# Kernel tuning notes

Hardware: AMD Instinct MI355X
Metric: run time of the kernel (lower is better)

## Reference

```python
import jax, jax.numpy as jnp
import numpy as np

N_NODES = 50000

def _sage_conv(x, src, dst, W_l, b_l, W_r):
    # PyG SAGEConv, aggr='mean': out = lin_l(mean_j x_j) + lin_r(x_i)
    msg = x[src]                                                 # [E, d] gather
    agg = jax.ops.segment_sum(msg, dst, num_segments=N_NODES)   # [N, d] scatter-add
    cnt = jax.ops.segment_sum(jnp.ones((src.shape[0], 1), x.dtype), dst,
                              num_segments=N_NODES)              # [N, 1] in-degree
    agg = agg / jnp.maximum(cnt, 1.0)                            # mean (0 for isolated nodes)
    return agg @ W_l + b_l + x @ W_r

def setup_inputs() -> dict:
    key = jax.random.key(0)
    ks = jax.random.split(key, 8)
    in_f, hid, out_f = 128, 128, 64
    E = 640000
    x = jax.random.normal(ks[0], (N_NODES, in_f), dtype=jnp.float32)
    edge_index = jax.random.randint(ks[1], (2, E), 0, N_NODES, dtype=jnp.int64)
    def glorot(k, fan_in, fan_out):
        lim = (6.0 / (fan_in + fan_out)) ** 0.5
        return jax.random.uniform(k, (fan_in, fan_out), jnp.float32, -lim, lim)
    return {
        "x": x,
        "edge_index": edge_index,
        "W1_l": glorot(ks[2], in_f, hid),
        "b1": jnp.zeros((hid,), jnp.float32),
        "W1_r": glorot(ks[3], in_f, hid),
        "W2_l": glorot(ks[4], hid, out_f),
        "b2": jnp.zeros((out_f,), jnp.float32),
        "W2_r": glorot(ks[5], hid, out_f),
    }

def reference(x, edge_index, W1_l, b1, W1_r, W2_l, b2, W2_r):
    src, dst = edge_index[0], edge_index[1]
    h = _sage_conv(x, src, dst, W1_l, b1, W1_r)
    h = jax.nn.relu(h)
    # dropout: eval mode -> identity (deterministic reference)
    h = _sage_conv(h, src, dst, W2_l, b2, W2_r)
    return h
```

## Files before the change

kernel.cpp:

```cpp
#include <hip/hip_runtime.h>
#include <cstddef>

static constexpr int N_NODES = 50000;
static constexpr int E_EDGES = 640000;
static constexpr int F = 128;
static constexpr int MAXD = 64;

typedef __bf16 b8 __attribute__((ext_vector_type(8)));
typedef float  f4 __attribute__((ext_vector_type(4)));
typedef float  f2 __attribute__((ext_vector_type(2)));

__device__ inline unsigned short f2bf(float f) {
    unsigned u = __float_as_uint(f);
    u += 0x7FFF + ((u >> 16) & 1);
    return (unsigned short)(u >> 16);
}
__device__ inline float bflo(unsigned u) { return __uint_as_float(u << 16); }
__device__ inline float bfhi(unsigned u) { return __uint_as_float(u & 0xFFFF0000u); }

__device__ inline void accq(float* s, uint2 u) {
    f2 p;
    p = __builtin_amdgcn_cvt_pk_f32_fp8(u.x, false); s[0] += p.x; s[1] += p.y;
    p = __builtin_amdgcn_cvt_pk_f32_fp8(u.x, true);  s[2] += p.x; s[3] += p.y;
    p = __builtin_amdgcn_cvt_pk_f32_fp8(u.y, false); s[4] += p.x; s[5] += p.y;
    p = __builtin_amdgcn_cvt_pk_f32_fp8(u.y, true);  s[6] += p.x; s[7] += p.y;
}
__device__ inline void accq16(float* s, uint4 u) {
    accq(s,     make_uint2(u.x, u.y));
    accq(s + 8, make_uint2(u.z, u.w));
}

template<int BN>
__device__ inline void pack_w_body(int t, const float* __restrict__ Wl,
                                   const float* __restrict__ Wr, uint4* __restrict__ Bp) {
    constexpr int NTg = BN / 16;
    int wid = t >> 6, lane = t & 63;
    if (wid >= 8 * NTg) return;
    int kq = lane >> 4, m = lane & 15;
    int kt = wid / NTg, nt = wid % NTg;
    unsigned short tmp[8];
#pragma unroll
    for (int j = 0; j < 8; ++j) {
        int k = kt * 32 + kq * 8 + j;
        const float* W = (k < 128) ? Wl : Wr;
        tmp[j] = f2bf(W[(size_t)(k & 127) * BN + nt * 16 + m]);
    }
    uint4 u;
    u.x = tmp[0] | ((unsigned)tmp[1] << 16);
    u.y = tmp[2] | ((unsigned)tmp[3] << 16);
    u.z = tmp[4] | ((unsigned)tmp[5] << 16);
    u.w = tmp[6] | ((unsigned)tmp[7] << 16);
    Bp[wid * 64 + lane] = u;
}

__global__ __launch_bounds__(256)
void prep(const int* __restrict__ ei, int* __restrict__ deg, int* __restrict__ col,
          const float* __restrict__ x, uint4* __restrict__ xb, uint2* __restrict__ xq,
          const float* __restrict__ W1l, const float* __restrict__ W1r, uint4* __restrict__ Bp1,
          const float* __restrict__ W2l, const float* __restrict__ W2r, uint4* __restrict__ Bp2) {
    int b = blockIdx.x, tid = threadIdx.x;
    if (b < 5000 && (b & 1) == 0) {
        int e = (b >> 1) * 256 + tid;
        int s = ei[e], d = ei[E_EDGES + e];
        int r = atomicAdd(&deg[d], 1);
        if (r < MAXD) col[(d << 6) + r] = s;
    } else if (b < 5625) {
        int ci = (b < 5000) ? (b >> 1) : (2500 + (b - 5000));
        int i = ci * 256 + tid;
        const float4* s = (const float4*)x + (size_t)i * 2;
        float4 v0 = s[0], v1 = s[1];
        uint4 u;
        u.x = f2bf(v0.x) | ((unsigned)f2bf(v0.y) << 16);
        u.y = f2bf(v0.z) | ((unsigned)f2bf(v0.w) << 16);
        u.z = f2bf(v1.x) | ((unsigned)f2bf(v1.y) << 16);
        u.w = f2bf(v1.z) | ((unsigned)f2bf(v1.w) << 16);
        xb[i] = u;
        uint2 q;
        q.x = __builtin_amdgcn_cvt_pk_fp8_f32(v0.x, v0.y, 0, false);
        q.x = __builtin_amdgcn_cvt_pk_fp8_f32(v0.z, v0.w, q.x, true);
        q.y = __builtin_amdgcn_cvt_pk_fp8_f32(v1.x, v1.y, 0, false);
        q.y = __builtin_amdgcn_cvt_pk_fp8_f32(v1.z, v1.w, q.y, true);
        xq[i] = q;
    } else if (b < 5641) {
        pack_w_body<128>((b - 5625) * 256 + tid, W1l, W1r, Bp1);
    } else {
        pack_w_body<64>((b - 5641) * 256 + tid, W2l, W2r, Bp2);
    }
}

__global__ __launch_bounds__(256)
void sage_l1(const uint2* __restrict__ featq,
             const unsigned short* __restrict__ featb,
             const int* __restrict__ deg,
             const int* __restrict__ col,
             const unsigned short* __restrict__ Bp1,
             const unsigned short* __restrict__ Bp2,
             const float* __restrict__ b1,
             const float* __restrict__ b2,
             unsigned char* __restrict__ Zq,
             float* __restrict__ out) {
    constexpr int LDW = 68;
    __shared__ unsigned Alds[16 * LDW];
    __shared__ unsigned short Hlds[16 * 136];

    const int tid  = threadIdx.x;
    const int wv   = tid >> 6;
    const int lane = tid & 63;
    const int c    = lane & 15;
    const int g    = lane >> 4;
    const int node0 = blockIdx.x * 16;
    const int node  = node0 + wv * 4 + g;

    {
        int d0 = deg[node];
        int d  = d0 < MAXD ? d0 : MAXD;
        int jb = node << 6, je = jb + d;
        float s0[8] = {0.f,0.f,0.f,0.f,0.f,0.f,0.f,0.f};
        float s1[8] = {0.f,0.f,0.f,0.f,0.f,0.f,0.f,0.f};
        float s2[8] = {0.f,0.f,0.f,0.f,0.f,0.f,0.f,0.f};
        float s3[8] = {0.f,0.f,0.f,0.f,0.f,0.f,0.f,0.f};
        int j = jb;
        for (; j + 7 < je; j += 8) {
            uint2 u0 = featq[(size_t)col[j + 0] * 16 + c];
            uint2 u1 = featq[(size_t)col[j + 1] * 16 + c];
            uint2 u2 = featq[(size_t)col[j + 2] * 16 + c];
            uint2 u3 = featq[(size_t)col[j + 3] * 16 + c];
            uint2 u4 = featq[(size_t)col[j + 4] * 16 + c];
            uint2 u5 = featq[(size_t)col[j + 5] * 16 + c];
            uint2 u6 = featq[(size_t)col[j + 6] * 16 + c];
            uint2 u7 = featq[(size_t)col[j + 7] * 16 + c];
            accq(s0, u0); accq(s1, u1); accq(s2, u2); accq(s3, u3);
            accq(s0, u4); accq(s1, u5); accq(s2, u6); accq(s3, u7);
        }
        if (j + 3 < je) {
            uint2 u0 = featq[(size_t)col[j + 0] * 16 + c];
            uint2 u1 = featq[(size_t)col[j + 1] * 16 + c];
            uint2 u2 = featq[(size_t)col[j + 2] * 16 + c];
            uint2 u3 = featq[(size_t)col[j + 3] * 16 + c];
            accq(s0, u0); accq(s1, u1); accq(s2, u2); accq(s3, u3);
            j += 4;
        }
        for (; j < je; ++j) {
            uint2 u0 = featq[(size_t)col[j] * 16 + c];
            accq(s0, u0);
        }
        float inv = 1.0f / (float)(d > 0 ? d : 1);
        float r[8];
#pragma unroll
        for (int k = 0; k < 8; ++k) r[k] = ((s0[k] + s1[k]) + (s2[k] + s3[k])) * inv;
        uint4 o;
        o.x = f2bf(r[0]) | ((unsigned)f2bf(r[1]) << 16);
        o.y = f2bf(r[2]) | ((unsigned)f2bf(r[3]) << 16);
        o.z = f2bf(r[4]) | ((unsigned)f2bf(r[5]) << 16);
        o.w = f2bf(r[6]) | ((unsigned)f2bf(r[7]) << 16);
        *((uint4*)&Alds[(wv * 4 + g) * LDW + c * 4]) = o;
    }
    __syncthreads();

    const int m  = lane & 15;
    const int kq = lane >> 4;
    const unsigned short* srow = featb + (size_t)(node0 + m) * F + kq * 8;

    f4 zero = {0.f, 0.f, 0.f, 0.f};
    f4 acc[2] = {zero, zero};
#pragma unroll
    for (int kt = 0; kt < 8; ++kt) {
        b8 a;
        if (kt < 4) a = *((const b8*)((const char*)Alds + m * 272 + kt * 64 + kq * 16));
        else        a = *((const b8*)(srow + (kt - 4) * 32));
#pragma unroll
        for (int t = 0; t < 2; ++t) {
            int nt = wv * 2 + t;
            b8 b = *((const b8*)(Bp1 + ((size_t)(kt * 8 + nt) * 64 + lane) * 8));
            acc[t] = __builtin_amdgcn_mfma_f32_16x16x32_bf16(a, b, acc[t], 0, 0, 0);
        }
    }
    {
        int rowb = kq * 4;
#pragma unroll
        for (int t = 0; t < 2; ++t) {
            int cc = (wv * 2 + t) * 16 + m;
            float bv = b1[cc];
#pragma unroll
            for (int r = 0; r < 4; ++r) {
                float v = fmaxf(acc[t][r] + bv, 0.0f);
                Hlds[(rowb + r) * 136 + cc] = f2bf(v);
            }
        }
    }
    __syncthreads();

    f4 accZ = zero, accS = zero;
#pragma unroll
    for (int kt = 0; kt < 4; ++kt) {
        b8 a = *((const b8*)((const char*)Hlds + m * 272 + kt * 64 + kq * 16));
        b8 bz = *((const b8*)(Bp2 + ((size_t)(kt * 4 + wv) * 64 + lane) * 8));
        b8 bs = *((const b8*)(Bp2 + ((size_t)((kt + 4) * 4 + wv) * 64 + lane) * 8));
        accZ = __builtin_amdgcn_mfma_f32_16x16x32_bf16(a, bz, accZ, 0, 0, 0);
        accS = __builtin_amdgcn_mfma_f32_16x16x32_bf16(a, bs, accS, 0, 0, 0);
    }
    {
        int rowg = node0 + kq * 4;
        int cc = wv * 16 + m;
        float bv = b2[cc];
#pragma unroll
        for (int r = 0; r < 4; ++r) {
            unsigned q = __builtin_amdgcn_cvt_pk_fp8_f32(accZ[r], accZ[r], 0, false);
            Zq[(size_t)(rowg + r) * 64 + cc] = (unsigned char)(q & 0xFF);
            out[(size_t)(rowg + r) * 64 + cc] = accS[r] + bv;
        }
    }
}

__global__ __launch_bounds__(256)
void gather_add(const uint4* __restrict__ Zq,
                const int* __restrict__ deg,
                const int* __restrict__ col,
                float* __restrict__ out, int N) {
    int t = blockIdx.x * 256 + threadIdx.x;
    int node = t >> 2;
    if (node >= N) return;
    int c = t & 3;

    int d0 = deg[node];
    int d  = d0 < MAXD ? d0 : MAXD;
    int jb = node << 6, je = jb + d;
    float s0[16] = {0.f,0.f,0.f,0.f,0.f,0.f,0.f,0.f,0.f,0.f,0.f,0.f,0.f,0.f,0.f,0.f};
    float s1[16] = {0.f,0.f,0.f,0.f,0.f,0.f,0.f,0.f,0.f,0.f,0.f,0.f,0.f,0.f,0.f,0.f};
    float s2[16] = {0.f,0.f,0.f,0.f,0.f,0.f,0.f,0.f,0.f,0.f,0.f,0.f,0.f,0.f,0.f,0.f};
    float s3[16] = {0.f,0.f,0.f,0.f,0.f,0.f,0.f,0.f,0.f,0.f,0.f,0.f,0.f,0.f,0.f,0.f};
    int j = jb;
    for (; j + 7 < je; j += 8) {
        uint4 u0 = Zq[(size_t)col[j + 0] * 4 + c];
        uint4 u1 = Zq[(size_t)col[j + 1] * 4 + c];
        uint4 u2 = Zq[(size_t)col[j + 2] * 4 + c];
        uint4 u3 = Zq[(size_t)col[j + 3] * 4 + c];
        uint4 u4 = Zq[(size_t)col[j + 4] * 4 + c];
        uint4 u5 = Zq[(size_t)col[j + 5] * 4 + c];
        uint4 u6 = Zq[(size_t)col[j + 6] * 4 + c];
        uint4 u7 = Zq[(size_t)col[j + 7] * 4 + c];
        accq16(s0, u0); accq16(s1, u1); accq16(s2, u2); accq16(s3, u3);
        accq16(s0, u4); accq16(s1, u5); accq16(s2, u6); accq16(s3, u7);
    }
    if (j + 3 < je) {
        uint4 u0 = Zq[(size_t)col[j + 0] * 4 + c];
        uint4 u1 = Zq[(size_t)col[j + 1] * 4 + c];
        uint4 u2 = Zq[(size_t)col[j + 2] * 4 + c];
        uint4 u3 = Zq[(size_t)col[j + 3] * 4 + c];
        accq16(s0, u0); accq16(s1, u1); accq16(s2, u2); accq16(s3, u3);
        j += 4;
    }
    for (; j < je; ++j) {
        uint4 u0 = Zq[(size_t)col[j] * 4 + c];
        accq16(s0, u0);
    }
    float inv = 1.0f / (float)(d > 0 ? d : 1);
    float* op = out + (size_t)node * 64 + c * 16;
#pragma unroll
    for (int q = 0; q < 4; ++q) {
        float4 o = *((float4*)(op + q * 4));
        o.x += ((s0[q*4+0] + s1[q*4+0]) + (s2[q*4+0] + s3[q*4+0])) * inv;
        o.y += ((s0[q*4+1] + s1[q*4+1]) + (s2[q*4+1] + s3[q*4+1])) * inv;
        o.z += ((s0[q*4+2] + s1[q*4+2]) + (s2[q*4+2] + s3[q*4+2])) * inv;
        o.w += ((s0[q*4+3] + s1[q*4+3]) + (s2[q*4+3] + s3[q*4+3])) * inv;
        *((float4*)(op + q * 4)) = o;
    }
}


extern "C" void kernel_launch(void* const* d_in, const int* in_sizes, int n_in,
                              void* d_out, int out_size, void* d_ws, size_t ws_size,
                              hipStream_t stream) {
    const float* x   = (const float*)d_in[0];
    const int*   ei  = (const int*)d_in[1];
    const float* W1l = (const float*)d_in[2];
    const float* b1  = (const float*)d_in[3];
    const float* W1r = (const float*)d_in[4];
    const float* W2l = (const float*)d_in[5];
    const float* b2  = (const float*)d_in[6];
    const float* W2r = (const float*)d_in[7];
    float* out = (float*)d_out;

    unsigned* Zq    = (unsigned*)d_ws;
    unsigned* xb    = Zq + (size_t)N_NODES * 16;
    unsigned* xq    = xb + (size_t)N_NODES * 64;
    unsigned* Bp1   = xq + (size_t)N_NODES * 32;
    unsigned* Bp2   = Bp1 + 16384;
    int* col        = (int*)(Bp2 + 8192);
    int* deg        = col + (size_t)N_NODES * MAXD;

    hipMemsetAsync(deg, 0, (size_t)N_NODES * sizeof(int), stream);

    prep<<<5649, 256, 0, stream>>>(ei, deg, col, x, (uint4*)xb, (uint2*)xq,
                                   W1l, W1r, (uint4*)Bp1, W2l, W2r, (uint4*)Bp2);

    sage_l1<<<N_NODES / 16, 256, 0, stream>>>(
        (const uint2*)xq, (const unsigned short*)xb, deg, col,
        (const unsigned short*)Bp1, (const unsigned short*)Bp2,
        b1, b2, (unsigned char*)Zq, out);

    gather_add<<<(N_NODES * 4 + 255) / 256, 256, 0, stream>>>(
        (const uint4*)Zq, deg, col, out, N_NODES);
}
```

Measured before the change: 171.0 us.

## Pad degree counters, batch edge atomics per thread, widen gather_add parallelism

Degree counters are now padded to one per 64 bytes (stride 16 ints) so concurrent atomics on neighboring nodes do not share cache lines. Each edge thread in prep now handles four edges, issuing all loads and then all atomics, and the prep grid is rebalanced to fit. gather_add uses 8 threads per node with 8-byte loads instead of 4 threads with 16-byte loads, which doubles thread-level parallelism for the latency-bound gather. The cost is a 16x larger degree buffer to memset and fewer bytes per load.

```diff
diff --git a/kernel.cpp b/kernel.cpp
--- a/kernel.cpp
+++ b/kernel.cpp
@@ -5,6 +5,7 @@
 static constexpr int E_EDGES = 640000;
 static constexpr int F = 128;
 static constexpr int MAXD = 64;
+static constexpr int DEGS = 16;
 
 typedef __bf16 b8 __attribute__((ext_vector_type(8)));
 typedef float  f4 __attribute__((ext_vector_type(4)));
@@ -15,8 +16,6 @@
     u += 0x7FFF + ((u >> 16) & 1);
     return (unsigned short)(u >> 16);
 }
-__device__ inline float bflo(unsigned u) { return __uint_as_float(u << 16); }
-__device__ inline float bfhi(unsigned u) { return __uint_as_float(u & 0xFFFF0000u); }
 
 __device__ inline void accq(float* s, uint2 u) {
     f2 p;
@@ -24,10 +23,6 @@
     p = __builtin_amdgcn_cvt_pk_f32_fp8(u.x, true);  s[2] += p.x; s[3] += p.y;
     p = __builtin_amdgcn_cvt_pk_f32_fp8(u.y, false); s[4] += p.x; s[5] += p.y;
     p = __builtin_amdgcn_cvt_pk_f32_fp8(u.y, true);  s[6] += p.x; s[7] += p.y;
-}
-__device__ inline void accq16(float* s, uint4 u) {
-    accq(s,     make_uint2(u.x, u.y));
-    accq(s + 8, make_uint2(u.z, u.w));
 }
 
 template<int BN>
@@ -59,32 +54,43 @@
           const float* __restrict__ W1l, const float* __restrict__ W1r, uint4* __restrict__ Bp1,
           const float* __restrict__ W2l, const float* __restrict__ W2r, uint4* __restrict__ Bp2) {
     int b = blockIdx.x, tid = threadIdx.x;
-    if (b < 5000 && (b & 1) == 0) {
-        int e = (b >> 1) * 256 + tid;
-        int s = ei[e], d = ei[E_EDGES + e];
-        int r = atomicAdd(&deg[d], 1);
-        if (r < MAXD) col[(d << 6) + r] = s;
-    } else if (b < 5625) {
-        int ci = (b < 5000) ? (b >> 1) : (2500 + (b - 5000));
-        int i = ci * 256 + tid;
-        const float4* s = (const float4*)x + (size_t)i * 2;
-        float4 v0 = s[0], v1 = s[1];
-        uint4 u;
-        u.x = f2bf(v0.x) | ((unsigned)f2bf(v0.y) << 16);
-        u.y = f2bf(v0.z) | ((unsigned)f2bf(v0.w) << 16);
-        u.z = f2bf(v1.x) | ((unsigned)f2bf(v1.y) << 16);
-        u.w = f2bf(v1.z) | ((unsigned)f2bf(v1.w) << 16);
-        xb[i] = u;
-        uint2 q;
-        q.x = __builtin_amdgcn_cvt_pk_fp8_f32(v0.x, v0.y, 0, false);
-        q.x = __builtin_amdgcn_cvt_pk_fp8_f32(v0.z, v0.w, q.x, true);
-        q.y = __builtin_amdgcn_cvt_pk_fp8_f32(v1.x, v1.y, 0, false);
-        q.y = __builtin_amdgcn_cvt_pk_fp8_f32(v1.z, v1.w, q.y, true);
-        xq[i] = q;
-    } else if (b < 5641) {
-        pack_w_body<128>((b - 5625) * 256 + tid, W1l, W1r, Bp1);
+    if (b < 1250 && (b & 1) == 0) {
+        int e0 = (b >> 1) * 1024 + tid;
+        int s[4], d[4], r[4];
+#pragma unroll
+        for (int i = 0; i < 4; ++i) {
+            s[i] = ei[e0 + i * 256];
+            d[i] = ei[E_EDGES + e0 + i * 256];
+        }
+#pragma unroll
+        for (int i = 0; i < 4; ++i)
+            r[i] = atomicAdd(&deg[d[i] * DEGS], 1);
+#pragma unroll
+        for (int i = 0; i < 4; ++i)
+            if (r[i] < MAXD) col[(d[i] << 6) + r[i]] = s[i];
     } else {
-        pack_w_body<64>((b - 5641) * 256 + tid, W2l, W2r, Bp2);
+        int o = (b < 1250) ? (b >> 1) : (625 + (b - 1250));
+        if (o < 3125) {
+            int i = o * 256 + tid;
+            const float4* s = (const float4*)x + (size_t)i * 2;
+            float4 v0 = s[0], v1 = s[1];
+            uint4 u;
+            u.x = f2bf(v0.x) | ((unsigned)f2bf(v0.y) << 16);
+            u.y = f2bf(v0.z) | ((unsigned)f2bf(v0.w) << 16);
+            u.z = f2bf(v1.x) | ((unsigned)f2bf(v1.y) << 16);
+            u.w = f2bf(v1.z) | ((unsigned)f2bf(v1.w) << 16);
+            xb[i] = u;
+            uint2 q;
+            q.x = __builtin_amdgcn_cvt_pk_fp8_f32(v0.x, v0.y, 0, false);
+            q.x = __builtin_amdgcn_cvt_pk_fp8_f32(v0.z, v0.w, q.x, true);
+            q.y = __builtin_amdgcn_cvt_pk_fp8_f32(v1.x, v1.y, 0, false);
+            q.y = __builtin_amdgcn_cvt_pk_fp8_f32(v1.z, v1.w, q.y, true);
+            xq[i] = q;
+        } else if (o < 3141) {
+            pack_w_body<128>((o - 3125) * 256 + tid, W1l, W1r, Bp1);
+        } else {
+            pack_w_body<64>((o - 3141) * 256 + tid, W2l, W2r, Bp2);
+        }
     }
 }
 
@@ -112,7 +118,7 @@
     const int node  = node0 + wv * 4 + g;
 
     {
-        int d0 = deg[node];
+        int d0 = deg[node * DEGS];
         int d  = d0 < MAXD ? d0 : MAXD;
         int jb = node << 6, je = jb + d;
         float s0[8] = {0.f,0.f,0.f,0.f,0.f,0.f,0.f,0.f};
@@ -213,51 +219,51 @@
 }
 
 __global__ __launch_bounds__(256)
-void gather_add(const uint4* __restrict__ Zq,
+void gather_add(const uint2* __restrict__ Zq,
                 const int* __restrict__ deg,
                 const int* __restrict__ col,
                 float* __restrict__ out, int N) {
     int t = blockIdx.x * 256 + threadIdx.x;
-    int node = t >> 2;
+    int node = t >> 3;
     if (node >= N) return;
-    int c = t & 3;
-
-    int d0 = deg[node];
+    int c = t & 7;
+
+    int d0 = deg[node * DEGS];
     int d  = d0 < MAXD ? d0 : MAXD;
     int jb = node << 6, je = jb + d;
-    float s0[16] = {0.f,0.f,0.f,0.f,0.f,0.f,0.f,0.f,0.f,0.f,0.f,0.f,0.f,0.f,0.f,0.f};
-    float s1[16] = {0.f,0.f,0.f,0.f,0.f,0.f,0.f,0.f,0.f,0.f,0.f,0.f,0.f,0.f,0.f,0.f};
-    float s2[16] = {0.f,0.f,0.f,0.f,0.f,0.f,0.f,0.f,0.f,0.f,0.f,0.f,0.f,0.f,0.f,0.f};
-    float s3[16] = {0.f,0.f,0.f,0.f,0.f,0.f,0.f,0.f,0.f,0.f,0.f,0.f,0.f,0.f,0.f,0.f};
+    float s0[8] = {0.f,0.f,0.f,0.f,0.f,0.f,0.f,0.f};
+    float s1[8] = {0.f,0.f,0.f,0.f,0.f,0.f,0.f,0.f};
+    float s2[8] = {0.f,0.f,0.f,0.f,0.f,0.f,0.f,0.f};
+    float s3[8] = {0.f,0.f,0.f,0.f,0.f,0.f,0.f,0.f};
     int j = jb;
     for (; j + 7 < je; j += 8) {
-        uint4 u0 = Zq[(size_t)col[j + 0] * 4 + c];
-        uint4 u1 = Zq[(size_t)col[j + 1] * 4 + c];
-        uint4 u2 = Zq[(size_t)col[j + 2] * 4 + c];
-        uint4 u3 = Zq[(size_t)col[j + 3] * 4 + c];
-        uint4 u4 = Zq[(size_t)col[j + 4] * 4 + c];
-        uint4 u5 = Zq[(size_t)col[j + 5] * 4 + c];
-        uint4 u6 = Zq[(size_t)col[j + 6] * 4 + c];
-        uint4 u7 = Zq[(size_t)col[j + 7] * 4 + c];
-        accq16(s0, u0); accq16(s1, u1); accq16(s2, u2); accq16(s3, u3);
-        accq16(s0, u4); accq16(s1, u5); accq16(s2, u6); accq16(s3, u7);
+        uint2 u0 = Zq[(size_t)col[j + 0] * 8 + c];
+        uint2 u1 = Zq[(size_t)col[j + 1] * 8 + c];
+        uint2 u2 = Zq[(size_t)col[j + 2] * 8 + c];
+        uint2 u3 = Zq[(size_t)col[j + 3] * 8 + c];
+        uint2 u4 = Zq[(size_t)col[j + 4] * 8 + c];
+        uint2 u5 = Zq[(size_t)col[j + 5] * 8 + c];
+        uint2 u6 = Zq[(size_t)col[j + 6] * 8 + c];
+        uint2 u7 = Zq[(size_t)col[j + 7] * 8 + c];
+        accq(s0, u0); accq(s1, u1); accq(s2, u2); accq(s3, u3);
+        accq(s0, u4); accq(s1, u5); accq(s2, u6); accq(s3, u7);
     }
     if (j + 3 < je) {
-        uint4 u0 = Zq[(size_t)col[j + 0] * 4 + c];
-        uint4 u1 = Zq[(size_t)col[j + 1] * 4 + c];
-        uint4 u2 = Zq[(size_t)col[j + 2] * 4 + c];
-        uint4 u3 = Zq[(size_t)col[j + 3] * 4 + c];
-        accq16(s0, u0); accq16(s1, u1); accq16(s2, u2); accq16(s3, u3);
+        uint2 u0 = Zq[(size_t)col[j + 0] * 8 + c];
+        uint2 u1 = Zq[(size_t)col[j + 1] * 8 + c];
+        uint2 u2 = Zq[(size_t)col[j + 2] * 8 + c];
+        uint2 u3 = Zq[(size_t)col[j + 3] * 8 + c];
+        accq(s0, u0); accq(s1, u1); accq(s2, u2); accq(s3, u3);
         j += 4;
     }
     for (; j < je; ++j) {
-        uint4 u0 = Zq[(size_t)col[j] * 4 + c];
-        accq16(s0, u0);
+        uint2 u0 = Zq[(size_t)col[j] * 8 + c];
+        accq(s0, u0);
     }
     float inv = 1.0f / (float)(d > 0 ? d : 1);
-    float* op = out + (size_t)node * 64 + c * 16;
-#pragma unroll
-    for (int q = 0; q < 4; ++q) {
+    float* op = out + (size_t)node * 64 + c * 8;
+#pragma unroll
+    for (int q = 0; q < 2; ++q) {
         float4 o = *((float4*)(op + q * 4));
         o.x += ((s0[q*4+0] + s1[q*4+0]) + (s2[q*4+0] + s3[q*4+0])) * inv;
         o.y += ((s0[q*4+1] + s1[q*4+1]) + (s2[q*4+1] + s3[q*4+1])) * inv;
@@ -289,9 +295,9 @@
     int* col        = (int*)(Bp2 + 8192);
     int* deg        = col + (size_t)N_NODES * MAXD;
 
-    hipMemsetAsync(deg, 0, (size_t)N_NODES * sizeof(int), stream);
-
-    prep<<<5649, 256, 0, stream>>>(ei, deg, col, x, (uint4*)xb, (uint2*)xq,
+    hipMemsetAsync(deg, 0, (size_t)N_NODES * DEGS * sizeof(int), stream);
+
+    prep<<<3774, 256, 0, stream>>>(ei, deg, col, x, (uint4*)xb, (uint2*)xq,
                                    W1l, W1r, (uint4*)Bp1, W2l, W2r, (uint4*)Bp2);
 
     sage_l1<<<N_NODES / 16, 256, 0, stream>>>(
@@ -299,6 +305,6 @@
         (const unsigned short*)Bp1, (const unsigned short*)Bp2,
         b1, b2, (unsigned char*)Zq, out);
 
-    gather_add<<<(N_NODES * 4 + 255) / 256, 256, 0, stream>>>(
-        (const uint4*)Zq, deg, col, out, N_NODES);
-}
+    gather_add<<<(N_NODES * 8 + 255) / 256, 256, 0, stream>>>(
+        (const uint2*)Zq, deg, col, out, N_NODES);
+}
```

Result: no change. 172.3 us (+0.8%).
